# Kernel tuning notes

Hardware: AMD Instinct MI355X
Metric: run time of the kernel (lower is better)

Reference implementation:

```python
import jax, jax.numpy as jnp
import numpy as np

B, H, W, C, N = 4, 64, 2650, 64, 680000
THR = 0.5  # model_cfg.FOREGROUND_THRESHOLD


def setup_inputs() -> dict:
    key = jax.random.key(0)
    k1, k2, k3, k4, k5, k6 = jax.random.split(key, 6)
    pts = jax.random.normal(k1, (N, 5), dtype=jnp.float32)
    bidx = jax.random.randint(k2, (N,), 0, B)
    points = pts.at[:, 0].set(bidx.astype(jnp.float32))  # col 0 = batch index
    ri_h = jax.random.randint(k3, (N, 1), 0, H)
    ri_w = jax.random.randint(k4, (N, 1), 0, W)
    ri_indices = jnp.concatenate([ri_h, ri_w], axis=1).astype(jnp.int32)
    seg_pred = jax.random.uniform(k5, (B, H, W), dtype=jnp.float32)
    range_features = jax.random.normal(k6, (B, C, H, W), dtype=jnp.float32)
    return {"points": points, "ri_indices": ri_indices,
            "seg_pred": seg_pred, "range_features": range_features}


def reference(points, ri_indices, seg_pred, range_features):
    # Fully-vectorized version of the per-batch loop: each point gathers its
    # range-image feature/seg score via a flat (b*H*W + r*W + c) index.
    Bn, Cc, Hh, Ww = range_features.shape
    feats_flat = jnp.transpose(range_features, (0, 2, 3, 1)).reshape(Bn * Hh * Ww, Cc)
    seg_flat = seg_pred.reshape(Bn * Hh * Ww)
    b = points[:, 0].astype(jnp.int32)
    flat_idx = b * (Hh * Ww) + ri_indices[:, 0].astype(jnp.int32) * Ww + ri_indices[:, 1].astype(jnp.int32)  # [N]
    mask = seg_flat[flat_idx] >= THR                    # foreground mask [N] bool
    point_feats = feats_flat[flat_idx]                  # [N, C] gather
    out = jnp.concatenate([points, point_feats], axis=1)  # [N, 5+C]
    # jit-compatible stand-in for boolean compaction: zero out background rows
    out = out * mask[:, None].astype(out.dtype)
    return out, mask
```

## Files before the change

### kernel.cpp

```cpp
#include <hip/hip_runtime.h>

#define B_   4
#define H_   64
#define W_   2650
#define C_   64
#define N_   680000
#define THR_ 0.5f
#define HW_  (H_ * W_)
#define W16_ 166
#define M2_  (B_ * H_ * W16_)
#define NB2_ (M2_ / 256)


__global__ void zero_kernel(int* __restrict__ p) {
    p[blockIdx.x * 256 + threadIdx.x] = 0;
}

__device__ __forceinline__ int bin_of(const float* pts, const int* ri, int i) {
    int b = (int)pts[(size_t)i * 5];
    int r = ri[i * 2];
    int c = ri[i * 2 + 1];
    return (b * H_ + r) * W16_ + (c >> 4);
}

__global__ void hist_kernel(const float* __restrict__ pts,
                            const int* __restrict__ ri,
                            int* __restrict__ binarr) {
    int i = blockIdx.x * 256 + threadIdx.x;
    if (i >= N_) return;
    atomicAdd(&binarr[bin_of(pts, ri, i)], 1);
}

__global__ void scan1_kernel(int* __restrict__ binarr, int* __restrict__ bsum) {
    __shared__ int lds[256];
    int t = threadIdx.x;
    int g = blockIdx.x * 256 + t;
    int v = binarr[g];
    lds[t] = v;
    __syncthreads();
    for (int off = 1; off < 256; off <<= 1) {
        int x = (t >= off) ? lds[t - off] : 0;
        __syncthreads();
        lds[t] += x;
        __syncthreads();
    }
    binarr[g] = lds[t] - v;
    if (t == 255) bsum[blockIdx.x] = lds[255];
}

__global__ void scan2_kernel(int* __restrict__ bsum) {
    __shared__ int lds[256];
    int t = threadIdx.x;
    int v = (t < NB2_) ? bsum[t] : 0;
    lds[t] = v;
    __syncthreads();
    for (int off = 1; off < 256; off <<= 1) {
        int x = (t >= off) ? lds[t - off] : 0;
        __syncthreads();
        lds[t] += x;
        __syncthreads();
    }
    if (t < NB2_) bsum[t] = lds[t] - v;
}

__global__ void scan3_kernel(int* __restrict__ binarr, const int* __restrict__ bsum) {
    int g = blockIdx.x * 256 + threadIdx.x;
    binarr[g] += bsum[blockIdx.x];
}

__global__ void scatter_kernel(const float* __restrict__ pts,
                               const int* __restrict__ ri,
                               const float* __restrict__ seg,
                               int* __restrict__ binarr,
                               int* __restrict__ perm) {
    int i = blockIdx.x * 256 + threadIdx.x;
    if (i >= N_) return;
    int b   = (int)pts[(size_t)i * 5];
    int r   = ri[i * 2];
    int c   = ri[i * 2 + 1];
    int bin = (b * H_ + r) * W16_ + (c >> 4);
    int m   = (seg[(size_t)b * HW_ + r * W_ + c] >= THR_) ? 1 : 0;
    int slot = atomicAdd(&binarr[bin], 1);
    perm[slot] = i | ((c & 15) << 20) | (m << 24);
}

__global__ __launch_bounds__(256) void gather_kernel(
    const float* __restrict__ pts,
    const float* __restrict__ feat,
    const int*   __restrict__ binarr,
    const int*   __restrict__ perm,
    float* __restrict__ out,
    float* __restrict__ mask_out)
{
    __shared__ float lds[4][64 * 17];
    const int lane  = threadIdx.x & 63;
    const int wslot = threadIdx.x >> 6;
    const int bin   = blockIdx.x * 4 + wslot;

    const int end   = binarr[bin];
    const int start = (bin == 0) ? 0 : binarr[bin - 1];
    if (start == end) return;

    const int b    = bin / (H_ * W16_);
    const int rem  = bin % (H_ * W16_);
    const int r    = rem / W16_;
    const int col0 = (rem % W16_) * 16;

    const size_t fbase = (size_t)(b * C_ + lane) * HW_ + (size_t)r * W_ + col0;
    float* dst = &lds[wslot][lane * 17];
    if (col0 + 16 <= W_) {
        const float2* s2 = (const float2*)(feat + fbase);
#pragma unroll
        for (int j = 0; j < 8; j++) {
            float2 v = s2[j];
            dst[2 * j] = v.x;
            dst[2 * j + 1] = v.y;
        }
    } else {
#pragma unroll
        for (int j = 0; j < 16; j++) {
            int col = col0 + j;
            if (col >= W_) col = W_ - 1;
            dst[j] = feat[(size_t)(b * C_ + lane) * HW_ + (size_t)r * W_ + col];
        }
    }

    for (int p = start; p < end; p++) {
        int rec = perm[p];
        int pt  = rec & 0xFFFFF;
        int c15 = (rec >> 20) & 15;
        float m = (float)((rec >> 24) & 1);
        float f = lds[wslot][lane * 17 + c15];

        size_t orow = (size_t)pt * 69;
        out[orow + 5 + lane] = f * m;
        if (lane < 5) out[orow + lane] = pts[(size_t)pt * 5 + lane] * m;
        if (lane == 0) mask_out[pt] = m;
    }
}

__global__ __launch_bounds__(256) void gather_fallback(
    const float* __restrict__ pts, const int* __restrict__ ri,
    const float* __restrict__ seg, const float* __restrict__ feat,
    float* __restrict__ out, float* __restrict__ mask_out)
{
    const int lane = threadIdx.x & 63;
    const int pt   = blockIdx.x * 4 + (threadIdx.x >> 6);
    if (pt >= N_) return;
    int b = (int)pts[(size_t)pt * 5];
    int r = ri[pt * 2], c = ri[pt * 2 + 1];
    int rc = r * W_ + c;
    float m = (seg[b * HW_ + rc] >= THR_) ? 1.0f : 0.0f;
    float f = feat[(size_t)b * (C_ * HW_) + (size_t)lane * HW_ + rc];
    size_t orow = (size_t)pt * 69;
    out[orow + 5 + lane] = f * m;
    if (lane < 5) out[orow + lane] = pts[(size_t)pt * 5 + lane] * m;
    if (lane == 0) mask_out[pt] = m;
}


extern "C" void kernel_launch(void* const* d_in, const int* in_sizes, int n_in,
                              void* d_out, int out_size, void* d_ws, size_t ws_size,
                              hipStream_t stream) {
    const float* points = (const float*)d_in[0];
    const int*   ri     = (const int*)  d_in[1];
    const float* seg    = (const float*)d_in[2];
    const float* feat   = (const float*)d_in[3];

    float* out      = (float*)d_out;
    float* mask_out = (float*)d_out + (size_t)N_ * 69;

    int* binarr = (int*)d_ws;
    int* bsum   = binarr + M2_;
    int* perm   = bsum + 256;
    const size_t needed = ((size_t)M2_ + 256 + N_) * sizeof(int);
    const bool use_sort = (ws_size >= needed);

    const int nblkN = (N_ + 255) / 256;

    if (use_sort) {
        zero_kernel   <<<NB2_,   256, 0, stream>>>(binarr);
        hist_kernel   <<<nblkN,  256, 0, stream>>>(points, ri, binarr);
        scan1_kernel  <<<NB2_,   256, 0, stream>>>(binarr, bsum);
        scan2_kernel  <<<1,      256, 0, stream>>>(bsum);
        scan3_kernel  <<<NB2_,   256, 0, stream>>>(binarr, bsum);
        scatter_kernel<<<nblkN,  256, 0, stream>>>(points, ri, seg, binarr, perm);
        gather_kernel <<<M2_ / 4, 256, 0, stream>>>(points, feat, binarr, perm,
                                                    out, mask_out);
    } else {
        gather_fallback<<<(N_ + 3) / 4, 256, 0, stream>>>(points, ri, seg, feat,
                                                          out, mask_out);
    }
}
```

Baseline: 486.6 us.

## Fuse three-pass scan into single-block scan and batch perm/point loads in gather

Replaces the three scan kernels with one single-block kernel where each thread serially sums and rewrites a 166-entry segment around an LDS scan, removing two launches and the bsum buffer. In the gather kernel, each wave loads up to 64 perm records at once and shares them via shuffles, and stages the 5 point columns per record into LDS cooperatively, instead of one dependent load per record per iteration. The single-block scan runs serial, poorly coalesced strided loads on one CU, which may cost more than the launches it saves.

```diff
diff --git a/kernel.cpp b/kernel.cpp
--- a/kernel.cpp
+++ b/kernel.cpp
@@ -10,6 +10,7 @@
 #define W16_ 166
 #define M2_  (B_ * H_ * W16_)
 #define NB2_ (M2_ / 256)
+#define SEG_ 166
 
 
 __global__ void zero_kernel(int* __restrict__ p) {
@@ -31,12 +32,14 @@
     atomicAdd(&binarr[bin_of(pts, ri, i)], 1);
 }
 
-__global__ void scan1_kernel(int* __restrict__ binarr, int* __restrict__ bsum) {
+__global__ void scan_fused_kernel(int* __restrict__ binarr) {
     __shared__ int lds[256];
-    int t = threadIdx.x;
-    int g = blockIdx.x * 256 + t;
-    int v = binarr[g];
-    lds[t] = v;
+    const int t = threadIdx.x;
+    const int base = t * SEG_;
+    int s = 0;
+#pragma unroll 4
+    for (int k = 0; k < SEG_; k++) s += binarr[base + k];
+    lds[t] = s;
     __syncthreads();
     for (int off = 1; off < 256; off <<= 1) {
         int x = (t >= off) ? lds[t - off] : 0;
@@ -44,28 +47,13 @@
         lds[t] += x;
         __syncthreads();
     }
-    binarr[g] = lds[t] - v;
-    if (t == 255) bsum[blockIdx.x] = lds[255];
-}
-
-__global__ void scan2_kernel(int* __restrict__ bsum) {
-    __shared__ int lds[256];
-    int t = threadIdx.x;
-    int v = (t < NB2_) ? bsum[t] : 0;
-    lds[t] = v;
-    __syncthreads();
-    for (int off = 1; off < 256; off <<= 1) {
-        int x = (t >= off) ? lds[t - off] : 0;
-        __syncthreads();
-        lds[t] += x;
-        __syncthreads();
+    int run = lds[t] - s;
+#pragma unroll 4
+    for (int k = 0; k < SEG_; k++) {
+        int v = binarr[base + k];
+        binarr[base + k] = run;
+        run += v;
     }
-    if (t < NB2_) bsum[t] = lds[t] - v;
-}
-
-__global__ void scan3_kernel(int* __restrict__ binarr, const int* __restrict__ bsum) {
-    int g = blockIdx.x * 256 + threadIdx.x;
-    binarr[g] += bsum[blockIdx.x];
 }
 
 __global__ void scatter_kernel(const float* __restrict__ pts,
@@ -93,6 +81,7 @@
     float* __restrict__ mask_out)
 {
     __shared__ float lds[4][64 * 17];
+    __shared__ float alds[4][64 * 5];
     const int lane  = threadIdx.x & 63;
     const int wslot = threadIdx.x >> 6;
     const int bin   = blockIdx.x * 4 + wslot;
@@ -105,6 +94,9 @@
     const int rem  = bin % (H_ * W16_);
     const int r    = rem / W16_;
     const int col0 = (rem % W16_) * 16;
+
+    int cnt = min(end - start, 64);
+    int rec_l = (lane < cnt) ? perm[start + lane] : 0;
 
     const size_t fbase = (size_t)(b * C_ + lane) * HW_ + (size_t)r * W_ + col0;
     float* dst = &lds[wslot][lane * 17];
@@ -125,17 +117,33 @@
         }
     }
 
-    for (int p = start; p < end; p++) {
-        int rec = perm[p];
-        int pt  = rec & 0xFFFFF;
-        int c15 = (rec >> 20) & 15;
-        float m = (float)((rec >> 24) & 1);
-        float f = lds[wslot][lane * 17 + c15];
-
-        size_t orow = (size_t)pt * 69;
-        out[orow + 5 + lane] = f * m;
-        if (lane < 5) out[orow + lane] = pts[(size_t)pt * 5 + lane] * m;
-        if (lane == 0) mask_out[pt] = m;
+    float* arow = alds[wslot];
+    int p0 = start;
+    for (;;) {
+        const int na = cnt * 5;
+        for (int rbase = 0; rbase < na; rbase += 64) {
+            int idx = rbase + lane;
+            int pj  = idx / 5;
+            int a   = idx - pj * 5;
+            int pjc = (idx < na) ? pj : 0;
+            int ptj = __shfl(rec_l, pjc) & 0xFFFFF;
+            if (idx < na) arow[idx] = pts[(size_t)ptj * 5 + a];
+        }
+#pragma unroll 4
+        for (int j = 0; j < cnt; j++) {
+            const int rec = __shfl(rec_l, j);
+            const int pt  = rec & 0xFFFFF;
+            const float m = (float)((rec >> 24) & 1);
+            const float f = dst[(rec >> 20) & 15];
+            const size_t orow = (size_t)pt * 69;
+            out[orow + 5 + lane] = f * m;
+            if (lane < 5) out[orow + lane] = arow[j * 5 + lane] * m;
+            if (lane == 0) mask_out[pt] = m;
+        }
+        p0 += cnt;
+        if (p0 >= end) break;
+        cnt = min(end - p0, 64);
+        rec_l = (lane < cnt) ? perm[p0 + lane] : 0;
     }
 }
 
@@ -171,22 +179,19 @@
     float* mask_out = (float*)d_out + (size_t)N_ * 69;
 
     int* binarr = (int*)d_ws;
-    int* bsum   = binarr + M2_;
-    int* perm   = bsum + 256;
-    const size_t needed = ((size_t)M2_ + 256 + N_) * sizeof(int);
+    int* perm   = binarr + M2_;
+    const size_t needed = ((size_t)M2_ + N_) * sizeof(int);
     const bool use_sort = (ws_size >= needed);
 
     const int nblkN = (N_ + 255) / 256;
 
     if (use_sort) {
-        zero_kernel   <<<NB2_,   256, 0, stream>>>(binarr);
-        hist_kernel   <<<nblkN,  256, 0, stream>>>(points, ri, binarr);
-        scan1_kernel  <<<NB2_,   256, 0, stream>>>(binarr, bsum);
-        scan2_kernel  <<<1,      256, 0, stream>>>(bsum);
-        scan3_kernel  <<<NB2_,   256, 0, stream>>>(binarr, bsum);
-        scatter_kernel<<<nblkN,  256, 0, stream>>>(points, ri, seg, binarr, perm);
-        gather_kernel <<<M2_ / 4, 256, 0, stream>>>(points, feat, binarr, perm,
-                                                    out, mask_out);
+        zero_kernel     <<<NB2_,   256, 0, stream>>>(binarr);
+        hist_kernel     <<<nblkN,  256, 0, stream>>>(points, ri, binarr);
+        scan_fused_kernel<<<1,     256, 0, stream>>>(binarr);
+        scatter_kernel  <<<nblkN,  256, 0, stream>>>(points, ri, seg, binarr, perm);
+        gather_kernel   <<<M2_ / 4, 256, 0, stream>>>(points, feat, binarr, perm,
+                                                      out, mask_out);
     } else {
         gather_fallback<<<(N_ + 3) / 4, 256, 0, stream>>>(points, ri, seg, feat,
                                                           out, mask_out);
```

Measured after the change: 494.2 us. No clear change (+1.6%).

## Widen gather windows to 32 columns and batch perm and point loads per wave

Applied to the files above, without the earlier changes.

The gather kernel now has each wavefront handle a 32-column window made of two adjacent 16-column bins. The wave loads up to 64 perm records at once and broadcasts them with shuffles, instead of doing a serial global load per point. The 5 point attributes for a batch of points are staged cooperatively into LDS, and the hist and scatter kernels read ri as int2. The aim is to cut the serialized per-point load latency and the number of wavefronts that stage features, at the cost of more LDS per block and more redundant feature loads for sparse windows.

```diff
diff --git a/kernel.cpp b/kernel.cpp
--- a/kernel.cpp
+++ b/kernel.cpp
@@ -10,17 +10,12 @@
 #define W16_ 166
 #define M2_  (B_ * H_ * W16_)
 #define NB2_ (M2_ / 256)
+#define W32_ 83
+#define M32_ (B_ * H_ * W32_)
 
 
 __global__ void zero_kernel(int* __restrict__ p) {
     p[blockIdx.x * 256 + threadIdx.x] = 0;
-}
-
-__device__ __forceinline__ int bin_of(const float* pts, const int* ri, int i) {
-    int b = (int)pts[(size_t)i * 5];
-    int r = ri[i * 2];
-    int c = ri[i * 2 + 1];
-    return (b * H_ + r) * W16_ + (c >> 4);
 }
 
 __global__ void hist_kernel(const float* __restrict__ pts,
@@ -28,7 +23,9 @@
                             int* __restrict__ binarr) {
     int i = blockIdx.x * 256 + threadIdx.x;
     if (i >= N_) return;
-    atomicAdd(&binarr[bin_of(pts, ri, i)], 1);
+    int b = (int)pts[(size_t)i * 5];
+    int2 rc = ((const int2*)ri)[i];
+    atomicAdd(&binarr[(b * H_ + rc.x) * W16_ + (rc.y >> 4)], 1);
 }
 
 __global__ void scan1_kernel(int* __restrict__ binarr, int* __restrict__ bsum) {
@@ -76,12 +73,12 @@
     int i = blockIdx.x * 256 + threadIdx.x;
     if (i >= N_) return;
     int b   = (int)pts[(size_t)i * 5];
-    int r   = ri[i * 2];
-    int c   = ri[i * 2 + 1];
+    int2 rc = ((const int2*)ri)[i];
+    int r = rc.x, c = rc.y;
     int bin = (b * H_ + r) * W16_ + (c >> 4);
     int m   = (seg[(size_t)b * HW_ + r * W_ + c] >= THR_) ? 1 : 0;
     int slot = atomicAdd(&binarr[bin], 1);
-    perm[slot] = i | ((c & 15) << 20) | (m << 24);
+    perm[slot] = i | ((c & 31) << 20) | (m << 25);
 }
 
 __global__ __launch_bounds__(256) void gather_kernel(
@@ -92,50 +89,70 @@
     float* __restrict__ out,
     float* __restrict__ mask_out)
 {
-    __shared__ float lds[4][64 * 17];
+    __shared__ float lds[4][64 * 34];
+    __shared__ float alds[4][64 * 5];
     const int lane  = threadIdx.x & 63;
     const int wslot = threadIdx.x >> 6;
-    const int bin   = blockIdx.x * 4 + wslot;
-
-    const int end   = binarr[bin];
-    const int start = (bin == 0) ? 0 : binarr[bin - 1];
+    const int win   = blockIdx.x * 4 + wslot;
+
+    const int end   = binarr[2 * win + 1];
+    const int start = (win == 0) ? 0 : binarr[2 * win - 1];
     if (start == end) return;
 
-    const int b    = bin / (H_ * W16_);
-    const int rem  = bin % (H_ * W16_);
-    const int r    = rem / W16_;
-    const int col0 = (rem % W16_) * 16;
+    const int b    = win / (H_ * W32_);
+    const int rem  = win % (H_ * W32_);
+    const int r    = rem / W32_;
+    const int col0 = (rem % W32_) * 32;
+
+    int cnt = min(end - start, 64);
+    int rec_l = (lane < cnt) ? perm[start + lane] : 0;
 
     const size_t fbase = (size_t)(b * C_ + lane) * HW_ + (size_t)r * W_ + col0;
-    float* dst = &lds[wslot][lane * 17];
-    if (col0 + 16 <= W_) {
+    float* dst = &lds[wslot][lane * 34];
+    if (col0 + 32 <= W_) {
         const float2* s2 = (const float2*)(feat + fbase);
 #pragma unroll
-        for (int j = 0; j < 8; j++) {
+        for (int j = 0; j < 16; j++) {
             float2 v = s2[j];
             dst[2 * j] = v.x;
             dst[2 * j + 1] = v.y;
         }
     } else {
 #pragma unroll
-        for (int j = 0; j < 16; j++) {
+        for (int j = 0; j < 32; j++) {
             int col = col0 + j;
             if (col >= W_) col = W_ - 1;
             dst[j] = feat[(size_t)(b * C_ + lane) * HW_ + (size_t)r * W_ + col];
         }
     }
 
-    for (int p = start; p < end; p++) {
-        int rec = perm[p];
-        int pt  = rec & 0xFFFFF;
-        int c15 = (rec >> 20) & 15;
-        float m = (float)((rec >> 24) & 1);
-        float f = lds[wslot][lane * 17 + c15];
-
-        size_t orow = (size_t)pt * 69;
-        out[orow + 5 + lane] = f * m;
-        if (lane < 5) out[orow + lane] = pts[(size_t)pt * 5 + lane] * m;
-        if (lane == 0) mask_out[pt] = m;
+    float* arow = alds[wslot];
+    int p0 = start;
+    for (;;) {
+        const int na = cnt * 5;
+        for (int rbase = 0; rbase < na; rbase += 64) {
+            int idx = rbase + lane;
+            int pj  = idx / 5;
+            int a   = idx - pj * 5;
+            int pjc = (idx < na) ? pj : 0;
+            int ptj = __shfl(rec_l, pjc) & 0xFFFFF;
+            if (idx < na) arow[idx] = pts[(size_t)ptj * 5 + a];
+        }
+#pragma unroll 4
+        for (int j = 0; j < cnt; j++) {
+            const int rec = __shfl(rec_l, j);
+            const int pt  = rec & 0xFFFFF;
+            const float m = (float)((rec >> 25) & 1);
+            const float f = dst[(rec >> 20) & 31];
+            const size_t orow = (size_t)pt * 69;
+            out[orow + 5 + lane] = f * m;
+            if (lane < 5) out[orow + lane] = arow[j * 5 + lane] * m;
+            if (lane == 0) mask_out[pt] = m;
+        }
+        p0 += cnt;
+        if (p0 >= end) break;
+        cnt = min(end - p0, 64);
+        rec_l = (lane < cnt) ? perm[p0 + lane] : 0;
     }
 }
 
@@ -179,14 +196,14 @@
     const int nblkN = (N_ + 255) / 256;
 
     if (use_sort) {
-        zero_kernel   <<<NB2_,   256, 0, stream>>>(binarr);
-        hist_kernel   <<<nblkN,  256, 0, stream>>>(points, ri, binarr);
-        scan1_kernel  <<<NB2_,   256, 0, stream>>>(binarr, bsum);
-        scan2_kernel  <<<1,      256, 0, stream>>>(bsum);
-        scan3_kernel  <<<NB2_,   256, 0, stream>>>(binarr, bsum);
-        scatter_kernel<<<nblkN,  256, 0, stream>>>(points, ri, seg, binarr, perm);
-        gather_kernel <<<M2_ / 4, 256, 0, stream>>>(points, feat, binarr, perm,
-                                                    out, mask_out);
+        zero_kernel   <<<NB2_,    256, 0, stream>>>(binarr);
+        hist_kernel   <<<nblkN,   256, 0, stream>>>(points, ri, binarr);
+        scan1_kernel  <<<NB2_,    256, 0, stream>>>(binarr, bsum);
+        scan2_kernel  <<<1,       256, 0, stream>>>(bsum);
+        scan3_kernel  <<<NB2_,    256, 0, stream>>>(binarr, bsum);
+        scatter_kernel<<<nblkN,   256, 0, stream>>>(points, ri, seg, binarr, perm);
+        gather_kernel <<<M32_ / 4, 256, 0, stream>>>(points, feat, binarr, perm,
+                                                     out, mask_out);
     } else {
         gather_fallback<<<(N_ + 3) / 4, 256, 0, stream>>>(points, ri, seg, feat,
                                                           out, mask_out);
```

After: 471.8 us. 3.1% less time.
